# Optimization experiments

Hardware: AMD Instinct MI355X
Metric: run time of the kernel (lower is better)

Reference implementation:

```python
import jax, jax.numpy as jnp
import numpy as np

B, N, FEAT, H, HID = 2, 2048, 128, 5, 3
D = H * HID  # 15
NEG_INF = -9e15


def _gat(x, adj, W, a, concat):
    # x: [B,N,Fin], W: [Fin,Fout], a: [2*Fout]
    Wh = jnp.einsum('bnf,fo->bno', x, W)
    Fo = W.shape[1]
    f1 = Wh @ a[:Fo]          # [B,N]
    f2 = Wh @ a[Fo:]          # [B,N]
    e = jax.nn.leaky_relu(f1[:, :, None] + f2[:, None, :], 0.2)  # [B,N,N]
    att = jax.nn.softmax(jnp.where(adj > 0, e, NEG_INF), axis=-1)
    h = jnp.einsum('bij,bjo->bio', att, Wh)
    return (jax.nn.elu(h) if concat else h), att


def _diff_pool(x, adj, s):
    # torch_geometric.dense_diff_pool
    s = jax.nn.softmax(s, axis=-1)                       # [B,N,K]
    out = jnp.einsum('bnk,bnf->bkf', s, x)               # [B,K,F]
    out_adj = jnp.einsum('bnk,bnm,bml->bkl', s, adj, s)  # [B,K,K]
    link = jnp.linalg.norm(adj - jnp.einsum('bnk,bmk->bnm', s, s)) / adj.size
    ent = jnp.mean(jnp.sum(-s * jnp.log(s + 1e-15), axis=-1))
    return out, out_adj, link, ent


def setup_inputs() -> dict:
    key = jax.random.key(0)
    ks = jax.random.split(key, 16)
    p = lambda k, shp: (jax.random.normal(k, shp, jnp.float32) * 0.1)
    d = {}
    d['x'] = jax.random.normal(ks[0], (B, N, FEAT), jnp.float32)
    d['adj'] = jax.random.bernoulli(ks[1], 0.05, (B, N, N)).astype(jnp.float32)
    d['W_heads'] = p(ks[2], (H, FEAT, HID))
    d['a_heads'] = p(ks[3], (H, 2 * HID))
    d['W_out'] = p(ks[4], (D, D)); d['a_out'] = p(ks[5], (2 * D,))
    d['W_p1'] = p(ks[6], (D, 32)); d['a_p1'] = p(ks[7], (64,))
    d['lin1_w'] = p(ks[8], (32, 32)); d['lin1_b'] = p(ks[9], (32,))
    d['W_p2'] = p(ks[10], (D, 4)); d['a_p2'] = p(ks[11], (8,))
    d['lin2_w'] = p(ks[12], (4, 4)); d['lin2_b'] = p(ks[13], (4,))
    d['lin_w'] = p(ks[14], (4 * D, 2)); d['lin_b'] = p(ks[15], (2,))
    return d


def reference(x, adj, W_heads, a_heads, W_out, a_out, W_p1, a_p1,
              lin1_w, lin1_b, W_p2, a_p2, lin2_w, lin2_b, lin_w, lin_b):
    # eval mode: dropout = identity
    hs, atts = jax.vmap(lambda W, a: _gat(x, adj, W, a, True))(W_heads, a_heads)
    # hs: [H,B,N,HID] -> concat heads -> [B,N,H*HID]
    h = jnp.moveaxis(hs, 0, 2).reshape(x.shape[0], x.shape[1], -1)
    h = jax.nn.elu(_gat(h, adj, W_out, a_out, False)[0])
    # pool 1: N -> 32 clusters
    s1 = _gat(h, adj, W_p1, a_p1, True)[0] @ lin1_w + lin1_b
    h, adj2, link1, ent1 = _diff_pool(h, adj, s1)
    # pool 2: 32 -> 4 clusters
    s2 = _gat(h, adj2, W_p2, a_p2, True)[0] @ lin2_w + lin2_b
    h, adj3, link2, ent2 = _diff_pool(h, adj2, s2)
    ypred = h.reshape(h.shape[0], -1) @ lin_w + lin_b  # [B, class_num]
    loss = link1 + link2
    return ypred, loss, atts
```

## Files before the change

kernel.cpp:

```cpp
#include <hip/hip_runtime.h>
#include <hip/hip_bf16.h>

#define NN 2048
#define BB 2
#define RB 4096
#define CAP 192

__device__ __forceinline__ float lrelu(float v) { return v > 0.f ? v : 0.2f * v; }
__device__ __forceinline__ float eluf(float v) { return v > 0.f ? v : __expf(v) - 1.f; }

__device__ __forceinline__ float wredsum(float v) {
    for (int o = 32; o; o >>= 1) v += __shfl_down(v, o, 64);
    return v;
}
__device__ __forceinline__ float bsum(float v) {
    for (int m = 32; m; m >>= 1) v += __shfl_xor(v, m, 64);
    return v;
}
__device__ __forceinline__ float bmax(float v) {
    for (int m = 32; m; m >>= 1) v = fmaxf(v, __shfl_xor(v, m, 64));
    return v;
}

__global__ __launch_bounds__(256) void k_prep1(const float* __restrict__ x,
                                               const float* __restrict__ W,
                                               const float* __restrict__ a,
                                               float* __restrict__ Wh1,
                                               float* __restrict__ f1o,
                                               float* __restrict__ f2o,
                                               float* __restrict__ S) {
    if (blockIdx.x == 0 && threadIdx.x < 2) S[threadIdx.x] = 0.f;
    const int tid = threadIdx.x, w = tid >> 6, lane = tid & 63;
    const int r = blockIdx.x * 4 + w;
    const float xa = x[(size_t)r * 128 + lane];
    const float xb = x[(size_t)r * 128 + 64 + lane];
#pragma unroll
    for (int h = 0; h < 5; ++h) {
        float f1v = 0.f, f2v = 0.f;
#pragma unroll
        for (int f = 0; f < 3; ++f) {
            const float w0 = W[h * 384 + lane * 3 + f];
            const float w1 = W[h * 384 + (lane + 64) * 3 + f];
            const float d = bsum(xa * w0 + xb * w1);
            if (lane == 0) Wh1[((size_t)h * RB + r) * 3 + f] = d;
            f1v += d * a[h * 6 + f];
            f2v += d * a[h * 6 + 3 + f];
        }
        if (lane == 0) { f1o[h * RB + r] = f1v; f2o[h * RB + r] = f2v; }
    }
}

__global__ __launch_bounds__(320) void k_gat1(const float* __restrict__ adj,
                                              const float* __restrict__ Wh,
                                              const float* __restrict__ f1,
                                              const float* __restrict__ f2,
                                              const float* __restrict__ W_out,
                                              const float* __restrict__ a_out,
                                              float* __restrict__ Wh2,
                                              float* __restrict__ f1_2,
                                              float* __restrict__ f2_2,
                                              float* __restrict__ att_out,
                                              int* __restrict__ nnzcnt,
                                              unsigned short* __restrict__ nnzidx,
                                              float* __restrict__ S) {
    __shared__ float dense[2052];
    __shared__ unsigned short nidx[CAP];
    __shared__ float h1row[15];
    __shared__ float f1l[5], invl[5];
    __shared__ int ncnt;
    const int tid = threadIdx.x, h = tid >> 6, lane = tid & 63;
    const int r = blockIdx.x;
    const int b = r >> 11, i = r & (NN - 1);
    const float* arow = adj + ((size_t)b * NN + i) * NN;

    if (tid == 0) ncnt = 0;
    __syncthreads();
    for (int it = 0; it < 7; ++it) {
        const int j = tid + it * 320;
        const bool p = (j < NN) && (arow[j] > 0.f);
        const unsigned long long bal = __ballot(p);
        const int cw = __popcll(bal);
        int base = 0;
        if (lane == 0 && cw) base = atomicAdd(&ncnt, cw);
        base = __shfl(base, 0);
        if (p) {
            const int pos = base + __popcll(bal & ((1ull << lane) - 1ull));
            if (pos < CAP) nidx[pos] = (unsigned short)j;
        }
    }
    __syncthreads();
    const int cnt = min(ncnt, CAP);
    if (tid == 0) { nnzcnt[r] = cnt; atomicAdd(S, (float)ncnt); }
    for (int p = tid; p < cnt; p += 320) nnzidx[(size_t)r * CAP + p] = nidx[p];
    float4* d4 = (float4*)dense;
    for (int s = tid; s < 513; s += 320) d4[s] = make_float4(0.f, 0.f, 0.f, 0.f);

    const float f1i = f1[h * RB + r];
    const float* f2h = f2 + h * RB + b * NN;
    const float* WhB = Wh + ((size_t)h * RB + b * NN) * 3;
    float lsum = 0.f, h0 = 0.f, h1v = 0.f, h2v = 0.f;
    for (int q = lane; q < cnt; q += 64) {
        const int j = nidx[q];
        const float p = __expf(lrelu(f1i + f2h[j]));
        lsum += p;
        const float* wv = WhB + (size_t)j * 3;
        h0 += p * wv[0]; h1v += p * wv[1]; h2v += p * wv[2];
    }
    const float inv = 1.f / bsum(lsum);
    h0 = bsum(h0); h1v = bsum(h1v); h2v = bsum(h2v);
    if (lane == 0) {
        f1l[h] = f1i; invl[h] = inv;
        h1row[h * 3 + 0] = eluf(h0 * inv);
        h1row[h * 3 + 1] = eluf(h1v * inv);
        h1row[h * 3 + 2] = eluf(h2v * inv);
    }
    __syncthreads();

    for (int hh = 0; hh < 5; ++hh) {
        const float f1v = f1l[hh], iv = invl[hh];
        const float* f2hh = f2 + hh * RB + b * NN;
        for (int q = tid; q < cnt; q += 320) {
            const int j = nidx[q];
            dense[j + 1] = __expf(lrelu(f1v + f2hh[j])) * iv;
        }
        __syncthreads();
        float* ao = att_out + (((size_t)hh * BB + b) * NN + i) * NN;
        float4* ao4 = (float4*)(ao + 3);
        for (int s = tid; s < 511; s += 320) {
            const float4 v = d4[1 + s];
            ao4[s] = v;
            d4[1 + s] = make_float4(0.f, 0.f, 0.f, 0.f);
        }
        if (tid == 311) {
            ao[0] = dense[1]; ao[1] = dense[2]; ao[2] = dense[3];
            d4[0] = make_float4(0.f, 0.f, 0.f, 0.f);
        } else if (tid == 312) {
            ao[2047] = dense[2048];
            d4[512] = make_float4(0.f, 0.f, 0.f, 0.f);
        }
        __syncthreads();
    }

    if (h == 0) {
        float whv = 0.f;
        if (lane < 15) {
#pragma unroll
            for (int f = 0; f < 15; f++) whv += h1row[f] * W_out[f * 15 + lane];
            Wh2[(size_t)r * 15 + lane] = whv;
        }
        float s1p = (lane < 15) ? whv * a_out[lane] : 0.f;
        float s2p = (lane < 15) ? whv * a_out[15 + lane] : 0.f;
        s1p = wredsum(s1p); s2p = wredsum(s2p);
        if (lane == 0) { f1_2[r] = s1p; f2_2[r] = s2p; }
    }
}

__global__ __launch_bounds__(256) void k_gat2(const int* __restrict__ nnzcnt,
                                              const unsigned short* __restrict__ nnzidx,
                                              const float* __restrict__ Wh2,
                                              const float* __restrict__ f1_2,
                                              const float* __restrict__ f2_2,
                                              const float* __restrict__ W_p1,
                                              const float* __restrict__ a_p1,
                                              float* __restrict__ h2,
                                              float* __restrict__ Wh3,
                                              float* __restrict__ f1_3,
                                              float* __restrict__ f2_3) {
    __shared__ unsigned short sidx[4][CAP];
    __shared__ float sp[4][CAP];
    __shared__ float h2l[4][15];
    const int tid = threadIdx.x, w = tid >> 6, lane = tid & 63;
    const int r = blockIdx.x * 4 + w;
    const int b = r >> 11;
    const int cnt = nnzcnt[r];
    for (int q = lane; q < cnt; q += 64) sidx[w][q] = nnzidx[(size_t)r * CAP + q];
    __syncthreads();

    const float f1i = f1_2[r];
    float ee[3];
    float lm = -3.0e38f;
#pragma unroll
    for (int t3 = 0; t3 < 3; ++t3) {
        const int q = lane + 64 * t3;
        if (q < cnt) {
            const int j = sidx[w][q];
            const float v = lrelu(f1i + f2_2[b * NN + j]);
            ee[t3] = v;
            lm = fmaxf(lm, v);
        } else ee[t3] = -3.0e38f;
    }
    const float m = bmax(lm);
    float lsum = 0.f;
#pragma unroll
    for (int t3 = 0; t3 < 3; ++t3) {
        const int q = lane + 64 * t3;
        if (q < cnt) {
            const float p = __expf(ee[t3] - m);
            sp[w][q] = p;
            lsum += p;
        }
    }
    const float inv = 1.f / bsum(lsum);
    __syncthreads();

    const int g4 = lane / 15, f = lane - g4 * 15;
    float acc = 0.f;
    if (lane < 60) {
        for (int q = g4; q < cnt; q += 4)
            acc += sp[w][q] * Wh2[(size_t)(b * NN + sidx[w][q]) * 15 + f];
    }
    acc += __shfl_down(acc, 15, 64);
    acc += __shfl_down(acc, 30, 64);
    if (lane < 15) {
        const float v = eluf(acc * inv);
        h2[(size_t)r * 15 + f] = v;
        h2l[w][f] = v;
    }
    __syncthreads();

    float wh3 = 0.f;
    if (lane < 32) {
#pragma unroll
        for (int ff = 0; ff < 15; ++ff) wh3 += h2l[w][ff] * W_p1[ff * 32 + lane];
        Wh3[(size_t)r * 32 + lane] = wh3;
    }
    float s1p = (lane < 32) ? wh3 * a_p1[lane] : 0.f;
    float s2p = (lane < 32) ? wh3 * a_p1[32 + lane] : 0.f;
    s1p = bsum(s1p); s2p = bsum(s2p);
    if (lane == 0) { f1_3[r] = s1p; f2_3[r] = s2p; }
}

__global__ __launch_bounds__(256) void k_gat3(const int* __restrict__ nnzcnt,
                                              const unsigned short* __restrict__ nnzidx,
                                              const float* __restrict__ Wh3,
                                              const float* __restrict__ f1_3,
                                              const float* __restrict__ f2_3,
                                              const float* __restrict__ lw,
                                              const float* __restrict__ lb,
                                              float* __restrict__ s_out) {
    __shared__ unsigned short sidx[4][CAP];
    __shared__ float sp[4][CAP];
    __shared__ float h3l[4][32];
    const int tid = threadIdx.x, w = tid >> 6, lane = tid & 63;
    const int r = blockIdx.x * 4 + w;
    const int b = r >> 11;
    const int cnt = nnzcnt[r];
    for (int q = lane; q < cnt; q += 64) sidx[w][q] = nnzidx[(size_t)r * CAP + q];
    __syncthreads();

    const float f1i = f1_3[r];
    float ee[3];
    float lm = -3.0e38f;
#pragma unroll
    for (int t3 = 0; t3 < 3; ++t3) {
        const int q = lane + 64 * t3;
        if (q < cnt) {
            const int j = sidx[w][q];
            const float v = lrelu(f1i + f2_3[b * NN + j]);
            ee[t3] = v;
            lm = fmaxf(lm, v);
        } else ee[t3] = -3.0e38f;
    }
    const float m = bmax(lm);
    float lsum = 0.f;
#pragma unroll
    for (int t3 = 0; t3 < 3; ++t3) {
        const int q = lane + 64 * t3;
        if (q < cnt) {
            const float p = __expf(ee[t3] - m);
            sp[w][q] = p;
            lsum += p;
        }
    }
    const float inv = 1.f / bsum(lsum);
    __syncthreads();

    const int g2 = lane >> 5, f = lane & 31;
    float acc = 0.f;
    for (int q = g2; q < cnt; q += 2)
        acc += sp[w][q] * Wh3[(size_t)(b * NN + sidx[w][q]) * 32 + f];
    acc += __shfl_xor(acc, 32, 64);
    if (lane < 32) h3l[w][f] = eluf(acc * inv);
    __syncthreads();

    float z = -3.0e38f;
    if (lane < 32) {
        z = lb[lane];
#pragma unroll
        for (int ff = 0; ff < 32; ++ff) z += h3l[w][ff] * lw[ff * 32 + lane];
    }
    const float zm = bmax(z);
    const float p2 = (lane < 32) ? __expf(z - zm) : 0.f;
    const float zinv = 1.f / bsum(p2);
    if (lane < 32) s_out[(size_t)r * 32 + lane] = p2 * zinv;
}

__global__ __launch_bounds__(256) void k_tsp(const int* __restrict__ nnzcnt,
                                             const unsigned short* __restrict__ nnzidx,
                                             const float* __restrict__ smat,
                                             float* __restrict__ t) {
    __shared__ unsigned short sidx[4][CAP];
    const int tid = threadIdx.x, w = tid >> 6, lane = tid & 63;
    const int r = blockIdx.x * 4 + w;
    const int b = r >> 11;
    const int cnt = nnzcnt[r];
    for (int q = lane; q < cnt; q += 64) sidx[w][q] = nnzidx[(size_t)r * CAP + q];
    __syncthreads();
    const int g2 = lane >> 5, f = lane & 31;
    float acc = 0.f;
    for (int q = g2; q < cnt; q += 2)
        acc += smat[(size_t)(b * NN + sidx[w][q]) * 32 + f];
    acc += __shfl_xor(acc, 32, 64);
    if (lane < 32) t[(size_t)r * 32 + f] = acc;
}

__global__ __launch_bounds__(256) void k_pstats(const float* __restrict__ s,
                                                const float* __restrict__ t,
                                                const float* __restrict__ h2,
                                                float* __restrict__ adj2,
                                                float* __restrict__ hp1,
                                                float* __restrict__ S) {
    const int bk = blockIdx.x;
    const int b = bk >> 5, k = bk & 31;
    const int tid = threadIdx.x, lane = tid & 63, wid = tid >> 6;
    __shared__ float redG[128], redT[128], redH[60];
    __shared__ float gsq[32], tval[32];
    float aG[32], aT[32], aH[15];
#pragma unroll
    for (int l = 0; l < 32; l++) { aG[l] = 0.f; aT[l] = 0.f; }
#pragma unroll
    for (int f = 0; f < 15; f++) aH[f] = 0.f;
    const float* sb = s + (size_t)b * NN * 32;
    const float* tb = t + (size_t)b * NN * 32;
    const float* hb = h2 + (size_t)b * NN * 15;
    for (int n = tid; n < NN; n += 256) {
        const float sv = sb[(size_t)n * 32 + k];
        const float* sj = sb + (size_t)n * 32;
        const float* tj = tb + (size_t)n * 32;
        const float* hj = hb + (size_t)n * 15;
#pragma unroll
        for (int l = 0; l < 32; l++) { aG[l] += sv * sj[l]; aT[l] += sv * tj[l]; }
#pragma unroll
        for (int f = 0; f < 15; f++) aH[f] += sv * hj[f];
    }
#pragma unroll
    for (int l = 0; l < 32; l++) {
        const float vG = wredsum(aG[l]);
        const float vT = wredsum(aT[l]);
        if (lane == 0) { redG[wid * 32 + l] = vG; redT[wid * 32 + l] = vT; }
    }
#pragma unroll
    for (int f = 0; f < 15; f++) {
        const float vH = wredsum(aH[f]);
        if (lane == 0) redH[wid * 15 + f] = vH;
    }
    __syncthreads();
    if (tid < 32) {
        const float G = redG[tid] + redG[32 + tid] + redG[64 + tid] + redG[96 + tid];
        const float T = redT[tid] + redT[32 + tid] + redT[64 + tid] + redT[96 + tid];
        adj2[((size_t)b * 32 + k) * 32 + tid] = T;
        gsq[tid] = G * G;
        tval[tid] = T;
    }
    if (tid < 15) hp1[((size_t)b * 32 + k) * 15 + tid] = redH[tid] + redH[15 + tid] + redH[30 + tid] + redH[45 + tid];
    __syncthreads();
    if (tid == 0) {
        float ss = 0.f;
#pragma unroll
        for (int l = 0; l < 32; l++) ss += gsq[l];
        atomicAdd(S, ss - 2.f * tval[k]);
    }
}

__global__ __launch_bounds__(64) void k_pool2(const float* __restrict__ hp1,
                                              const float* __restrict__ adj2,
                                              const float* __restrict__ Wp2, const float* __restrict__ a2,
                                              const float* __restrict__ l2w, const float* __restrict__ l2b,
                                              const float* __restrict__ lw, const float* __restrict__ lb,
                                              const float* __restrict__ S, float* __restrict__ out) {
    __shared__ float hp[480], a2l[1024], wh[128], f1l[32], f2l[32], s2l[128], hp2[60];
    const int tid = threadIdx.x;
    float link2 = 0.f;
    for (int b = 0; b < BB; ++b) {
        __syncthreads();
        for (int idx = tid; idx < 480; idx += 64) hp[idx] = hp1[b * 480 + idx];
        for (int idx = tid; idx < 1024; idx += 64) a2l[idx] = adj2[b * 1024 + idx];
        __syncthreads();
        for (int idx = tid; idx < 128; idx += 64) {
            const int n = idx >> 2, c = idx & 3;
            float acc = 0.f;
#pragma unroll
            for (int f = 0; f < 15; f++) acc += hp[n * 15 + f] * Wp2[f * 4 + c];
            wh[idx] = acc;
        }
        __syncthreads();
        if (tid < 32) {
            float s1 = 0.f, s2 = 0.f;
#pragma unroll
            for (int c = 0; c < 4; c++) {
                s1 += wh[tid * 4 + c] * a2[c];
                s2 += wh[tid * 4 + c] * a2[4 + c];
            }
            f1l[tid] = s1;
            f2l[tid] = s2;
        }
        __syncthreads();
        if (tid < 32) {
            const int n = tid;
            float e[32];
            float m = -3.0e38f;
#pragma unroll
            for (int j = 0; j < 32; j++) {
                const float v = lrelu(f1l[n] + f2l[j]);
                e[j] = a2l[n * 32 + j] > 0.f ? v : -9.0e15f;
                m = fmaxf(m, e[j]);
            }
            float sum = 0.f;
#pragma unroll
            for (int j = 0; j < 32; j++) { e[j] = __expf(e[j] - m); sum += e[j]; }
            const float inv = 1.f / sum;
            float h4[4];
#pragma unroll
            for (int c = 0; c < 4; c++) {
                float acc = 0.f;
#pragma unroll
                for (int j = 0; j < 32; j++) acc += e[j] * wh[j * 4 + c];
                h4[c] = eluf(acc * inv);
            }
            float z[4];
            float zm = -3.0e38f;
#pragma unroll
            for (int c = 0; c < 4; c++) {
                float acc = l2b[c];
#pragma unroll
                for (int c2 = 0; c2 < 4; c2++) acc += h4[c2] * l2w[c2 * 4 + c];
                z[c] = acc;
                zm = fmaxf(zm, acc);
            }
            float zs = 0.f;
#pragma unroll
            for (int c = 0; c < 4; c++) { z[c] = __expf(z[c] - zm); zs += z[c]; }
            const float zi = 1.f / zs;
#pragma unroll
            for (int c = 0; c < 4; c++) s2l[n * 4 + c] = z[c] * zi;
        }
        __syncthreads();
        if (tid < 60) {
            const int c = tid / 15, f = tid % 15;
            float acc = 0.f;
#pragma unroll
            for (int n = 0; n < 32; n++) acc += s2l[n * 4 + c] * hp[n * 15 + f];
            hp2[tid] = acc;
        }
        float lacc = 0.f;
        for (int idx = tid; idx < 1024; idx += 64) {
            const int n = idx >> 5, mm = idx & 31;
            float d = 0.f;
#pragma unroll
            for (int c = 0; c < 4; c++) d += s2l[n * 4 + c] * s2l[mm * 4 + c];
            const float df = a2l[idx] - d;
            lacc += df * df;
        }
        lacc = wredsum(lacc);
        link2 += lacc;
        __syncthreads();
        if (tid < 2) {
            float acc = lb[tid];
#pragma unroll
            for (int k2 = 0; k2 < 60; k2++) acc += hp2[k2] * lw[k2 * 2 + tid];
            out[b * 2 + tid] = acc;
        }
    }
    if (tid == 0) out[4] = sqrtf(S[0]) / 8388608.f + sqrtf(link2) / 2048.f;
}

extern "C" void kernel_launch(void* const* d_in, const int* in_sizes, int n_in,
                              void* d_out, int out_size, void* d_ws, size_t ws_size,
                              hipStream_t stream) {
    const float* x      = (const float*)d_in[0];
    const float* adj    = (const float*)d_in[1];
    const float* W_h    = (const float*)d_in[2];
    const float* a_h    = (const float*)d_in[3];
    const float* W_out  = (const float*)d_in[4];
    const float* a_out  = (const float*)d_in[5];
    const float* W_p1   = (const float*)d_in[6];
    const float* a_p1   = (const float*)d_in[7];
    const float* lin1_w = (const float*)d_in[8];
    const float* lin1_b = (const float*)d_in[9];
    const float* W_p2   = (const float*)d_in[10];
    const float* a_p2   = (const float*)d_in[11];
    const float* lin2_w = (const float*)d_in[12];
    const float* lin2_b = (const float*)d_in[13];
    const float* lin_w  = (const float*)d_in[14];
    const float* lin_b  = (const float*)d_in[15];
    float* outp = (float*)d_out;

    float* W = (float*)d_ws;
    float* Wh1  = W;
    float* f1_1 = Wh1 + 61440;
    float* f2_1 = f1_1 + 20480;
    float* Wh2  = f2_1 + 20480;
    float* f1_2 = Wh2 + 61440;
    float* f2_2 = f1_2 + 4096;
    float* h2   = f2_2 + 4096;
    float* Wh3  = h2 + 61440;
    float* f1_3 = Wh3 + 131072;
    float* f2_3 = f1_3 + 4096;
    float* s    = f2_3 + 4096;
    float* t    = s + 131072;
    float* hp1  = t + 131072;
    float* adj2 = hp1 + 960;
    float* S    = adj2 + 2048;
    int* nnzcnt = (int*)(S + 2);
    unsigned short* nnzidx = (unsigned short*)(nnzcnt + RB);

    k_prep1<<<RB / 4, 256, 0, stream>>>(x, W_h, a_h, Wh1, f1_1, f2_1, S);
    k_gat1<<<RB, 320, 0, stream>>>(adj, Wh1, f1_1, f2_1, W_out, a_out,
                                   Wh2, f1_2, f2_2, outp + 5, nnzcnt, nnzidx, S);
    k_gat2<<<RB / 4, 256, 0, stream>>>(nnzcnt, nnzidx, Wh2, f1_2, f2_2,
                                       W_p1, a_p1, h2, Wh3, f1_3, f2_3);
    k_gat3<<<RB / 4, 256, 0, stream>>>(nnzcnt, nnzidx, Wh3, f1_3, f2_3,
                                       lin1_w, lin1_b, s);
    k_tsp<<<RB / 4, 256, 0, stream>>>(nnzcnt, nnzidx, s, t);
    k_pstats<<<64, 256, 0, stream>>>(s, t, h2, adj2, hp1, S);
    k_pool2<<<1, 64, 0, stream>>>(hp1, adj2, W_p2, a_p2, lin2_w, lin2_b, lin_w, lin_b, S, outp);
}
```

Measured before the change: 185.5 us.

## Split dense attention output writes across later small kernels to overlap work

```diff
diff --git a/kernel.cpp b/kernel.cpp
--- a/kernel.cpp
+++ b/kernel.cpp
@@ -50,7 +50,7 @@
     }
 }
 
-__global__ __launch_bounds__(320) void k_gat1(const float* __restrict__ adj,
+__global__ __launch_bounds__(320) void k_gata(const float* __restrict__ adj,
                                               const float* __restrict__ Wh,
                                               const float* __restrict__ f1,
                                               const float* __restrict__ f2,
@@ -59,14 +59,12 @@
                                               float* __restrict__ Wh2,
                                               float* __restrict__ f1_2,
                                               float* __restrict__ f2_2,
-                                              float* __restrict__ att_out,
+                                              float* __restrict__ sinv,
                                               int* __restrict__ nnzcnt,
                                               unsigned short* __restrict__ nnzidx,
                                               float* __restrict__ S) {
-    __shared__ float dense[2052];
     __shared__ unsigned short nidx[CAP];
     __shared__ float h1row[15];
-    __shared__ float f1l[5], invl[5];
     __shared__ int ncnt;
     const int tid = threadIdx.x, h = tid >> 6, lane = tid & 63;
     const int r = blockIdx.x;
@@ -92,8 +90,6 @@
     const int cnt = min(ncnt, CAP);
     if (tid == 0) { nnzcnt[r] = cnt; atomicAdd(S, (float)ncnt); }
     for (int p = tid; p < cnt; p += 320) nnzidx[(size_t)r * CAP + p] = nidx[p];
-    float4* d4 = (float4*)dense;
-    for (int s = tid; s < 513; s += 320) d4[s] = make_float4(0.f, 0.f, 0.f, 0.f);
 
     const float f1i = f1[h * RB + r];
     const float* f2h = f2 + h * RB + b * NN;
@@ -109,38 +105,12 @@
     const float inv = 1.f / bsum(lsum);
     h0 = bsum(h0); h1v = bsum(h1v); h2v = bsum(h2v);
     if (lane == 0) {
-        f1l[h] = f1i; invl[h] = inv;
+        sinv[h * RB + r] = inv;
         h1row[h * 3 + 0] = eluf(h0 * inv);
         h1row[h * 3 + 1] = eluf(h1v * inv);
         h1row[h * 3 + 2] = eluf(h2v * inv);
     }
     __syncthreads();
-
-    for (int hh = 0; hh < 5; ++hh) {
-        const float f1v = f1l[hh], iv = invl[hh];
-        const float* f2hh = f2 + hh * RB + b * NN;
-        for (int q = tid; q < cnt; q += 320) {
-            const int j = nidx[q];
-            dense[j + 1] = __expf(lrelu(f1v + f2hh[j])) * iv;
-        }
-        __syncthreads();
-        float* ao = att_out + (((size_t)hh * BB + b) * NN + i) * NN;
-        float4* ao4 = (float4*)(ao + 3);
-        for (int s = tid; s < 511; s += 320) {
-            const float4 v = d4[1 + s];
-            ao4[s] = v;
-            d4[1 + s] = make_float4(0.f, 0.f, 0.f, 0.f);
-        }
-        if (tid == 311) {
-            ao[0] = dense[1]; ao[1] = dense[2]; ao[2] = dense[3];
-            d4[0] = make_float4(0.f, 0.f, 0.f, 0.f);
-        } else if (tid == 312) {
-            ao[2047] = dense[2048];
-            d4[512] = make_float4(0.f, 0.f, 0.f, 0.f);
-        }
-        __syncthreads();
-    }
-
     if (h == 0) {
         float whv = 0.f;
         if (lane < 15) {
@@ -155,22 +125,53 @@
     }
 }
 
-__global__ __launch_bounds__(256) void k_gat2(const int* __restrict__ nnzcnt,
-                                              const unsigned short* __restrict__ nnzidx,
-                                              const float* __restrict__ Wh2,
-                                              const float* __restrict__ f1_2,
-                                              const float* __restrict__ f2_2,
-                                              const float* __restrict__ W_p1,
-                                              const float* __restrict__ a_p1,
-                                              float* __restrict__ h2,
-                                              float* __restrict__ Wh3,
-                                              float* __restrict__ f1_3,
-                                              float* __restrict__ f2_3) {
+__device__ __forceinline__ void dev_wrow(int hr,
+                                         const float* __restrict__ f1,
+                                         const float* __restrict__ f2,
+                                         const float* __restrict__ sinv,
+                                         const int* __restrict__ nnzcnt,
+                                         const unsigned short* __restrict__ nnzidx,
+                                         float* __restrict__ att_out) {
+    __shared__ float dense[2052];
+    const int tid = threadIdx.x;
+    const int h = hr >> 12, r = hr & (RB - 1);
+    const int b = r >> 11, i = r & (NN - 1);
+    float4* d4 = (float4*)dense;
+    for (int s2 = tid; s2 < 513; s2 += 256) d4[s2] = make_float4(0.f, 0.f, 0.f, 0.f);
+    __syncthreads();
+    const int cnt = nnzcnt[r];
+    const float f1i = f1[hr];
+    const float inv = sinv[hr];
+    const float* f2h = f2 + (hr - i);
+    for (int q = tid; q < cnt; q += 256) {
+        const int j = nnzidx[(size_t)r * CAP + q];
+        dense[j + 1] = __expf(lrelu(f1i + f2h[j])) * inv;
+    }
+    __syncthreads();
+    float* ao = att_out + (((size_t)h * BB + b) * NN + i) * NN;
+    float4* ao4 = (float4*)(ao + 3);
+    for (int s2 = tid; s2 < 511; s2 += 256) ao4[s2] = d4[1 + s2];
+    if (tid == 254) { ao[0] = dense[1]; ao[1] = dense[2]; ao[2] = dense[3]; }
+    if (tid == 255) ao[2047] = dense[2048];
+}
+
+__device__ __forceinline__ void dev_gat2(int blk,
+                                         const int* __restrict__ nnzcnt,
+                                         const unsigned short* __restrict__ nnzidx,
+                                         const float* __restrict__ Wh2,
+                                         const float* __restrict__ f1_2,
+                                         const float* __restrict__ f2_2,
+                                         const float* __restrict__ W_p1,
+                                         const float* __restrict__ a_p1,
+                                         float* __restrict__ h2,
+                                         float* __restrict__ Wh3,
+                                         float* __restrict__ f1_3,
+                                         float* __restrict__ f2_3) {
     __shared__ unsigned short sidx[4][CAP];
     __shared__ float sp[4][CAP];
     __shared__ float h2l[4][15];
     const int tid = threadIdx.x, w = tid >> 6, lane = tid & 63;
-    const int r = blockIdx.x * 4 + w;
+    const int r = blk * 4 + w;
     const int b = r >> 11;
     const int cnt = nnzcnt[r];
     for (int q = lane; q < cnt; q += 64) sidx[w][q] = nnzidx[(size_t)r * CAP + q];
@@ -230,19 +231,20 @@
     if (lane == 0) { f1_3[r] = s1p; f2_3[r] = s2p; }
 }
 
-__global__ __launch_bounds__(256) void k_gat3(const int* __restrict__ nnzcnt,
-                                              const unsigned short* __restrict__ nnzidx,
-                                              const float* __restrict__ Wh3,
-                                              const float* __restrict__ f1_3,
-                                              const float* __restrict__ f2_3,
-                                              const float* __restrict__ lw,
-                                              const float* __restrict__ lb,
-                                              float* __restrict__ s_out) {
+__device__ __forceinline__ void dev_gat3(int blk,
+                                         const int* __restrict__ nnzcnt,
+                                         const unsigned short* __restrict__ nnzidx,
+                                         const float* __restrict__ Wh3,
+                                         const float* __restrict__ f1_3,
+                                         const float* __restrict__ f2_3,
+                                         const float* __restrict__ lw,
+                                         const float* __restrict__ lb,
+                                         float* __restrict__ s_out) {
     __shared__ unsigned short sidx[4][CAP];
     __shared__ float sp[4][CAP];
     __shared__ float h3l[4][32];
     const int tid = threadIdx.x, w = tid >> 6, lane = tid & 63;
-    const int r = blockIdx.x * 4 + w;
+    const int r = blk * 4 + w;
     const int b = r >> 11;
     const int cnt = nnzcnt[r];
     for (int q = lane; q < cnt; q += 64) sidx[w][q] = nnzidx[(size_t)r * CAP + q];
@@ -295,13 +297,14 @@
     if (lane < 32) s_out[(size_t)r * 32 + lane] = p2 * zinv;
 }
 
-__global__ __launch_bounds__(256) void k_tsp(const int* __restrict__ nnzcnt,
-                                             const unsigned short* __restrict__ nnzidx,
-                                             const float* __restrict__ smat,
-                                             float* __restrict__ t) {
+__device__ __forceinline__ void dev_tsp(int blk,
+                                        const int* __restrict__ nnzcnt,
+                                        const unsigned short* __restrict__ nnzidx,
+                                        const float* __restrict__ smat,
+                                        float* __restrict__ t) {
     __shared__ unsigned short sidx[4][CAP];
     const int tid = threadIdx.x, w = tid >> 6, lane = tid & 63;
-    const int r = blockIdx.x * 4 + w;
+    const int r = blk * 4 + w;
     const int b = r >> 11;
     const int cnt = nnzcnt[r];
     for (int q = lane; q < cnt; q += 64) sidx[w][q] = nnzidx[(size_t)r * CAP + q];
@@ -314,14 +317,14 @@
     if (lane < 32) t[(size_t)r * 32 + f] = acc;
 }
 
-__global__ __launch_bounds__(256) void k_pstats(const float* __restrict__ s,
-                                                const float* __restrict__ t,
-                                                const float* __restrict__ h2,
-                                                float* __restrict__ adj2,
-                                                float* __restrict__ hp1,
-                                                float* __restrict__ S) {
-    const int bk = blockIdx.x;
-    const int b = bk >> 5, k = bk & 31;
+__device__ __forceinline__ void dev_pstats(int blk,
+                                           const float* __restrict__ s,
+                                           const float* __restrict__ t,
+                                           const float* __restrict__ h2,
+                                           float* __restrict__ adj2,
+                                           float* __restrict__ hp1,
+                                           float* __restrict__ S) {
+    const int b = blk >> 5, k = blk & 31;
     const int tid = threadIdx.x, lane = tid & 63, wid = tid >> 6;
     __shared__ float redG[128], redT[128], redH[60];
     __shared__ float gsq[32], tval[32];
@@ -370,6 +373,50 @@
         for (int l = 0; l < 32; l++) ss += gsq[l];
         atomicAdd(S, ss - 2.f * tval[k]);
     }
+}
+
+__global__ __launch_bounds__(256) void k_cmb_gat2(const int* nnzcnt, const unsigned short* nnzidx,
+                                                  const float* Wh2, const float* f1_2, const float* f2_2,
+                                                  const float* W_p1, const float* a_p1,
+                                                  float* h2, float* Wh3, float* f1_3, float* f2_3,
+                                                  const float* f1, const float* f2, const float* sinv,
+                                                  float* att, int wbase) {
+    if ((int)blockIdx.x < RB / 4)
+        dev_gat2(blockIdx.x, nnzcnt, nnzidx, Wh2, f1_2, f2_2, W_p1, a_p1, h2, Wh3, f1_3, f2_3);
+    else
+        dev_wrow(wbase + (int)blockIdx.x - RB / 4, f1, f2, sinv, nnzcnt, nnzidx, att);
+}
+
+__global__ __launch_bounds__(256) void k_cmb_gat3(const int* nnzcnt, const unsigned short* nnzidx,
+                                                  const float* Wh3, const float* f1_3, const float* f2_3,
+                                                  const float* lw, const float* lb, float* s_out,
+                                                  const float* f1, const float* f2, const float* sinv,
+                                                  float* att, int wbase) {
+    if ((int)blockIdx.x < RB / 4)
+        dev_gat3(blockIdx.x, nnzcnt, nnzidx, Wh3, f1_3, f2_3, lw, lb, s_out);
+    else
+        dev_wrow(wbase + (int)blockIdx.x - RB / 4, f1, f2, sinv, nnzcnt, nnzidx, att);
+}
+
+__global__ __launch_bounds__(256) void k_cmb_tsp(const int* nnzcnt, const unsigned short* nnzidx,
+                                                 const float* smat, float* t,
+                                                 const float* f1, const float* f2, const float* sinv,
+                                                 float* att, int wbase) {
+    if ((int)blockIdx.x < RB / 4)
+        dev_tsp(blockIdx.x, nnzcnt, nnzidx, smat, t);
+    else
+        dev_wrow(wbase + (int)blockIdx.x - RB / 4, f1, f2, sinv, nnzcnt, nnzidx, att);
+}
+
+__global__ __launch_bounds__(256) void k_cmb_pst(const float* s, const float* t, const float* h2,
+                                                 float* adj2, float* hp1, float* S,
+                                                 const int* nnzcnt, const unsigned short* nnzidx,
+                                                 const float* f1, const float* f2, const float* sinv,
+                                                 float* att, int wbase) {
+    if ((int)blockIdx.x < 64)
+        dev_pstats(blockIdx.x, s, t, h2, adj2, hp1, S);
+    else
+        dev_wrow(wbase + (int)blockIdx.x - 64, f1, f2, sinv, nnzcnt, nnzidx, att);
 }
 
 __global__ __launch_bounds__(64) void k_pool2(const float* __restrict__ hp1,
@@ -511,17 +558,25 @@
     float* hp1  = t + 131072;
     float* adj2 = hp1 + 960;
     float* S    = adj2 + 2048;
-    int* nnzcnt = (int*)(S + 2);
+    float* sinv = S + 2;
+    int* nnzcnt = (int*)(sinv + 20480);
     unsigned short* nnzidx = (unsigned short*)(nnzcnt + RB);
 
+    float* att = outp + 5;
+    const int WCHUNK = 5 * RB / 4;
+
     k_prep1<<<RB / 4, 256, 0, stream>>>(x, W_h, a_h, Wh1, f1_1, f2_1, S);
-    k_gat1<<<RB, 320, 0, stream>>>(adj, Wh1, f1_1, f2_1, W_out, a_out,
-                                   Wh2, f1_2, f2_2, outp + 5, nnzcnt, nnzidx, S);
-    k_gat2<<<RB / 4, 256, 0, stream>>>(nnzcnt, nnzidx, Wh2, f1_2, f2_2,
-                                       W_p1, a_p1, h2, Wh3, f1_3, f2_3);
-    k_gat3<<<RB / 4, 256, 0, stream>>>(nnzcnt, nnzidx, Wh3, f1_3, f2_3,
-                                       lin1_w, lin1_b, s);
-    k_tsp<<<RB / 4, 256, 0, stream>>>(nnzcnt, nnzidx, s, t);
-    k_pstats<<<64, 256, 0, stream>>>(s, t, h2, adj2, hp1, S);
+    k_gata<<<RB, 320, 0, stream>>>(adj, Wh1, f1_1, f2_1, W_out, a_out,
+                                   Wh2, f1_2, f2_2, sinv, nnzcnt, nnzidx, S);
+    k_cmb_gat2<<<RB / 4 + WCHUNK, 256, 0, stream>>>(nnzcnt, nnzidx, Wh2, f1_2, f2_2,
+                                                    W_p1, a_p1, h2, Wh3, f1_3, f2_3,
+                                                    f1_1, f2_1, sinv, att, 0 * WCHUNK);
+    k_cmb_gat3<<<RB / 4 + WCHUNK, 256, 0, stream>>>(nnzcnt, nnzidx, Wh3, f1_3, f2_3,
+                                                    lin1_w, lin1_b, s,
+                                                    f1_1, f2_1, sinv, att, 1 * WCHUNK);
+    k_cmb_tsp<<<RB / 4 + WCHUNK, 256, 0, stream>>>(nnzcnt, nnzidx, s, t,
+                                                   f1_1, f2_1, sinv, att, 2 * WCHUNK);
+    k_cmb_pst<<<64 + WCHUNK, 256, 0, stream>>>(s, t, h2, adj2, hp1, S,
+                                               nnzcnt, nnzidx, f1_1, f2_1, sinv, att, 3 * WCHUNK);
     k_pool2<<<1, 64, 0, stream>>>(hp1, adj2, W_p2, a_p2, lin2_w, lin2_b, lin_w, lin_b, S, outp);
 }
```

Measured after the change: 191.7 us. +3.3%, slower.

## Write attention rows per-warp from a shared bitmask instead of dense LDS staging

Applied to the files above, without the earlier changes.

```diff
diff --git a/kernel.cpp b/kernel.cpp
--- a/kernel.cpp
+++ b/kernel.cpp
@@ -63,10 +63,9 @@
                                               int* __restrict__ nnzcnt,
                                               unsigned short* __restrict__ nnzidx,
                                               float* __restrict__ S) {
-    __shared__ float dense[2052];
     __shared__ unsigned short nidx[CAP];
+    __shared__ unsigned int mask[64];
     __shared__ float h1row[15];
-    __shared__ float f1l[5], invl[5];
     __shared__ int ncnt;
     const int tid = threadIdx.x, h = tid >> 6, lane = tid & 63;
     const int r = blockIdx.x;
@@ -79,6 +78,10 @@
         const int j = tid + it * 320;
         const bool p = (j < NN) && (arow[j] > 0.f);
         const unsigned long long bal = __ballot(p);
+        if (j < NN) {
+            if (lane == 0)  mask[j >> 5] = (unsigned int)bal;
+            if (lane == 32) mask[j >> 5] = (unsigned int)(bal >> 32);
+        }
         const int cw = __popcll(bal);
         int base = 0;
         if (lane == 0 && cw) base = atomicAdd(&ncnt, cw);
@@ -92,8 +95,6 @@
     const int cnt = min(ncnt, CAP);
     if (tid == 0) { nnzcnt[r] = cnt; atomicAdd(S, (float)ncnt); }
     for (int p = tid; p < cnt; p += 320) nnzidx[(size_t)r * CAP + p] = nidx[p];
-    float4* d4 = (float4*)dense;
-    for (int s = tid; s < 513; s += 320) d4[s] = make_float4(0.f, 0.f, 0.f, 0.f);
 
     const float f1i = f1[h * RB + r];
     const float* f2h = f2 + h * RB + b * NN;
@@ -109,38 +110,41 @@
     const float inv = 1.f / bsum(lsum);
     h0 = bsum(h0); h1v = bsum(h1v); h2v = bsum(h2v);
     if (lane == 0) {
-        f1l[h] = f1i; invl[h] = inv;
         h1row[h * 3 + 0] = eluf(h0 * inv);
         h1row[h * 3 + 1] = eluf(h1v * inv);
         h1row[h * 3 + 2] = eluf(h2v * inv);
     }
-    __syncthreads();
-
-    for (int hh = 0; hh < 5; ++hh) {
-        const float f1v = f1l[hh], iv = invl[hh];
-        const float* f2hh = f2 + hh * RB + b * NN;
-        for (int q = tid; q < cnt; q += 320) {
-            const int j = nidx[q];
-            dense[j + 1] = __expf(lrelu(f1v + f2hh[j])) * iv;
-        }
-        __syncthreads();
-        float* ao = att_out + (((size_t)hh * BB + b) * NN + i) * NN;
-        float4* ao4 = (float4*)(ao + 3);
-        for (int s = tid; s < 511; s += 320) {
-            const float4 v = d4[1 + s];
-            ao4[s] = v;
-            d4[1 + s] = make_float4(0.f, 0.f, 0.f, 0.f);
-        }
-        if (tid == 311) {
-            ao[0] = dense[1]; ao[1] = dense[2]; ao[2] = dense[3];
-            d4[0] = make_float4(0.f, 0.f, 0.f, 0.f);
-        } else if (tid == 312) {
-            ao[2047] = dense[2048];
-            d4[512] = make_float4(0.f, 0.f, 0.f, 0.f);
-        }
-        __syncthreads();
-    }
-
+
+    #define MBIT(J) ((mask[(J) >> 5] >> ((J) & 31)) & 1u)
+    #define EVAL(J) (__expf(lrelu(f1i + f2h[(J)])) * inv)
+    float4 vals[8];
+#pragma unroll
+    for (int it = 0; it < 8; ++it) {
+        const int v = lane + 64 * it;
+        const int j0 = 3 + 4 * v;
+        float4 o = make_float4(0.f, 0.f, 0.f, 0.f);
+        o.x = MBIT(j0) ? EVAL(j0) : 0.f;
+        if (v < 511) {
+            o.y = MBIT(j0 + 1) ? EVAL(j0 + 1) : 0.f;
+            o.z = MBIT(j0 + 2) ? EVAL(j0 + 2) : 0.f;
+            o.w = MBIT(j0 + 3) ? EVAL(j0 + 3) : 0.f;
+        }
+        vals[it] = o;
+    }
+    float edge = 0.f;
+    if (lane < 3) edge = MBIT(lane) ? EVAL(lane) : 0.f;
+    #undef MBIT
+    #undef EVAL
+
+    float* ao = att_out + (((size_t)h * BB + b) * NN + i) * NN;
+    float4* ao4 = (float4*)(ao + 3);
+    if (lane < 3) ao[lane] = edge;
+#pragma unroll
+    for (int it = 0; it < 7; ++it) ao4[lane + 64 * it] = vals[it];
+    if (lane < 63) ao4[lane + 448] = vals[7];
+    else ao[2047] = vals[7].x;
+
+    __syncthreads();
     if (h == 0) {
         float whv = 0.f;
         if (lane < 15) {
```

Result: slower. 195.7 us (+5.5%).
